# Kernel optimization log

Hardware: AMD Instinct MI355X
Metric: run time of the kernel (lower is better)

The kernel has to match this reference:

```python
import jax, jax.numpy as jnp
import numpy as np

WEIGHT = 0.01

def setup_inputs() -> dict:
    key = jax.random.key(0)
    k1, k2 = jax.random.split(key)
    shape = jax.random.normal(k1, (16, 4096, 3), dtype=jnp.float32)
    template = jax.random.normal(k2, (16, 4096, 3), dtype=jnp.float32)
    return {"shape": shape, "template": template}

def _chamfer(pred, target):
    # Euclidean cdist via the |x|^2 + |y|^2 - 2<x,y> expansion to avoid a (B,M,N,3) tensor.
    p2 = jnp.sum(pred * pred, axis=-1)          # (B, M)
    t2 = jnp.sum(target * target, axis=-1)      # (B, N)
    cross = jnp.einsum('bmd,bnd->bmn', pred, target)  # (B, M, N)
    d2 = p2[:, :, None] + t2[None if p2.ndim == 1 else slice(None), None, :] - 2.0 * cross
    dist = jnp.sqrt(jnp.maximum(d2, 0.0))       # (B, M, N) euclidean, matches torch.cdist
    min_p2t = jnp.min(dist, axis=2)             # (B, M)
    min_t2p = jnp.min(dist, axis=1)             # (B, N)
    chamfer = jnp.sum(min_p2t, axis=1) + jnp.sum(min_t2p, axis=1)  # (B,)
    return jnp.mean(chamfer)                    # reduction='mean'

def reference(shape, template):
    return WEIGHT * _chamfer(shape, template)
```

## Files before the change

kernel.cpp:

```cpp
#include <hip/hip_runtime.h>

#define NPTS 4096
#define NBATCH 16
#define THREADS 256
#define QPB 128
#define TCH 1024
#define NCH (NPTS / TCH)

typedef __attribute__((ext_vector_type(8))) short short8;
typedef __attribute__((ext_vector_type(16))) float float16v;

static __device__ __forceinline__ unsigned short f2bf(float f) {
  unsigned int u = __builtin_bit_cast(unsigned int, f);
  u = (u + 0x7FFFu + ((u >> 16) & 1u)) >> 16;
  return (unsigned short)u;
}
static __device__ __forceinline__ float bf2f(unsigned short h) {
  unsigned int u = ((unsigned int)h) << 16;
  return __builtin_bit_cast(float, u);
}
static __device__ __forceinline__ int toff(int j, int h) {
  return (j * 16 + h * 8) ^ (((j >> 2) & 7) << 3);
}

__global__ __launch_bounds__(THREADS)
__attribute__((amdgpu_waves_per_eu(4, 4)))
void chamfer_mfma(const float* __restrict__ shape,
                  const float* __restrict__ tmpl,
                  float* __restrict__ out) {
  __shared__ unsigned short tgt[TCH * 16];
  __shared__ unsigned short qry[QPB * 16];
  __shared__ float redbuf[4];

  const int qc = blockIdx.x;
  const int b = blockIdx.y;
  const int dir = blockIdx.z;
  const float* Pb = (dir == 0 ? shape : tmpl) + (size_t)b * NPTS * 3;
  const float* Tb = (dir == 0 ? tmpl : shape) + (size_t)b * NPTS * 3;

  const int tid = threadIdx.x;
  const int lane = tid & 63;
  const int wave = tid >> 6;
  const int n = lane & 31;
  const int kg = lane >> 5;

  if (tid < QPB) {
    const int qg = qc * QPB + tid;
    const float px = Pb[3 * qg + 0], py = Pb[3 * qg + 1], pz = Pb[3 * qg + 2];
    const float ux = -2.0f * px, uy = -2.0f * py, uz = -2.0f * pz;
    const float p2 = fmaf(px, px, fmaf(py, py, pz * pz));
    const unsigned short hx = f2bf(ux), hy = f2bf(uy), hz = f2bf(uz);
    const unsigned short lx = f2bf(ux - bf2f(hx)), ly = f2bf(uy - bf2f(hy)),
                         lz = f2bf(uz - bf2f(hz));
    const unsigned short h2 = f2bf(p2), l2 = f2bf(p2 - bf2f(h2));
    const unsigned short ONE = 0x3F80;
    short8 v0, v1;
    v0[0] = hx; v0[1] = hx; v0[2] = lx; v0[3] = hy;
    v0[4] = hy; v0[5] = ly; v0[6] = hz; v0[7] = hz;
    v1[0] = lz; v1[1] = ONE; v1[2] = ONE; v1[3] = h2;
    v1[4] = l2; v1[5] = 0;  v1[6] = 0;  v1[7] = 0;
    *(short8*)&qry[tid * 16] = v0;
    *(short8*)&qry[tid * 16 + 8] = v1;
  }
  __syncthreads();

  const short8 af = *(const short8*)&qry[(wave * 32 + n) * 16 + kg * 8];

  const float INF = 3.402823466e38f;
  float acc[16];
  #pragma unroll
  for (int r = 0; r < 16; ++r) acc[r] = INF;
  const float16v z = {};

  const float4* T4 = (const float4*)Tb;
  for (int ch = 0; ch < NCH; ++ch) {
    __syncthreads();
    {
      const int g = ch * (TCH / 4) + tid;
      const float4 a = T4[g * 3 + 0];
      const float4 c = T4[g * 3 + 1];
      const float4 d = T4[g * 3 + 2];
      const float X[4] = {a.x, a.w, c.z, d.y};
      const float Y[4] = {a.y, c.x, c.w, d.z};
      const float Z[4] = {a.z, c.y, d.x, d.w};
      #pragma unroll
      for (int p = 0; p < 4; ++p) {
        const float x = X[p], y = Y[p], zc = Z[p];
        const float t2 = fmaf(x, x, fmaf(y, y, zc * zc));
        const unsigned short hx = f2bf(x), hy = f2bf(y), hz = f2bf(zc);
        const unsigned short lx = f2bf(x - bf2f(hx)), ly = f2bf(y - bf2f(hy)),
                             lz = f2bf(zc - bf2f(hz));
        const unsigned short h2 = f2bf(t2), l2 = f2bf(t2 - bf2f(h2));
        const unsigned short ONE = 0x3F80;
        short8 v0, v1;
        v0[0] = hx; v0[1] = lx; v0[2] = hx; v0[3] = hy;
        v0[4] = ly; v0[5] = hy; v0[6] = hz; v0[7] = lz;
        v1[0] = hz; v1[1] = h2; v1[2] = l2; v1[3] = ONE;
        v1[4] = ONE; v1[5] = 0; v1[6] = 0; v1[7] = 0;
        const int j = tid * 4 + p;
        *(short8*)&tgt[toff(j, 0)] = v0;
        *(short8*)&tgt[toff(j, 1)] = v1;
      }
    }
    __syncthreads();

    for (int tp = 0; tp < TCH / 64; ++tp) {
      const short8 b0 = *(const short8*)&tgt[toff(tp * 64 + n, kg)];
      const short8 b1 = *(const short8*)&tgt[toff(tp * 64 + 32 + n, kg)];
      float16v d0 = __builtin_amdgcn_mfma_f32_32x32x16_bf16(af, b0, z, 0, 0, 0);
      float16v d1 = __builtin_amdgcn_mfma_f32_32x32x16_bf16(af, b1, z, 0, 0, 0);
      #pragma unroll
      for (int r = 0; r < 16; ++r)
        acc[r] = fminf(fminf(d0[r], d1[r]), acc[r]);
    }
  }

  #pragma unroll
  for (int m = 1; m <= 16; m <<= 1) {
    #pragma unroll
    for (int r = 0; r < 16; ++r)
      acc[r] = fminf(acc[r], __shfl_xor(acc[r], m, 64));
  }

  float s = 0.0f;
  if (n == 0) {
    #pragma unroll
    for (int r = 0; r < 16; ++r)
      s += sqrtf(fmaxf(acc[r], 0.0f));
  }
  s += __shfl_xor(s, 32, 64);
  if (lane == 0) redbuf[wave] = s;
  __syncthreads();
  if (tid == 0) {
    atomicAdd(out, (redbuf[0] + redbuf[1] + redbuf[2] + redbuf[3]) * (0.01f / 16.0f));
  }
}

extern "C" void kernel_launch(void* const* d_in, const int* in_sizes, int n_in,
                              void* d_out, int out_size, void* d_ws, size_t ws_size,
                              hipStream_t stream) {
  const float* shape = (const float*)d_in[0];
  const float* tmpl = (const float*)d_in[1];
  float* out = (float*)d_out;

  hipMemsetAsync(out, 0, sizeof(float) * out_size, stream);

  dim3 grid(NPTS / QPB, NBATCH, 2);
  chamfer_mfma<<<grid, dim3(THREADS), 0, stream>>>(shape, tmpl, out);
}
```

Before: 80.94 us.

## Double queries per wave and split targets across blocks with a finish kernel

Each wave now handles 64 queries with two A fragments, so each B fragment read from LDS feeds four MFMAs instead of two. The target set is split into two halves across grid z, which keeps the block count the same as before. Partial per-query minima are written to workspace and a second kernel combines the halves, takes sqrt and reduces. This trades a second launch, extra global traffic and more accumulator registers for better LDS reuse and less B-conversion work per block.

New measurement: 82.86 us. 2.4% more time.

```diff
diff --git a/kernel.cpp b/kernel.cpp
--- a/kernel.cpp
+++ b/kernel.cpp
@@ -3,9 +3,10 @@
 #define NPTS 4096
 #define NBATCH 16
 #define THREADS 256
-#define QPB 128
+#define QPB 256
+#define TPB 2048
 #define TCH 1024
-#define NCH (NPTS / TCH)
+#define NCH (TPB / TCH)
 
 typedef __attribute__((ext_vector_type(8))) short short8;
 typedef __attribute__((ext_vector_type(16))) float float16v;
@@ -27,14 +28,14 @@
 __attribute__((amdgpu_waves_per_eu(4, 4)))
 void chamfer_mfma(const float* __restrict__ shape,
                   const float* __restrict__ tmpl,
-                  float* __restrict__ out) {
+                  float* __restrict__ ws) {
   __shared__ unsigned short tgt[TCH * 16];
   __shared__ unsigned short qry[QPB * 16];
-  __shared__ float redbuf[4];
 
   const int qc = blockIdx.x;
   const int b = blockIdx.y;
-  const int dir = blockIdx.z;
+  const int dir = blockIdx.z & 1;
+  const int tc = blockIdx.z >> 1;
   const float* Pb = (dir == 0 ? shape : tmpl) + (size_t)b * NPTS * 3;
   const float* Tb = (dir == 0 ? tmpl : shape) + (size_t)b * NPTS * 3;
 
@@ -44,7 +45,7 @@
   const int n = lane & 31;
   const int kg = lane >> 5;
 
-  if (tid < QPB) {
+  {
     const int qg = qc * QPB + tid;
     const float px = Pb[3 * qg + 0], py = Pb[3 * qg + 1], pz = Pb[3 * qg + 2];
     const float ux = -2.0f * px, uy = -2.0f * py, uz = -2.0f * pz;
@@ -64,19 +65,20 @@
   }
   __syncthreads();
 
-  const short8 af = *(const short8*)&qry[(wave * 32 + n) * 16 + kg * 8];
+  const short8 af0 = *(const short8*)&qry[(wave * 64 + n) * 16 + kg * 8];
+  const short8 af1 = *(const short8*)&qry[(wave * 64 + 32 + n) * 16 + kg * 8];
 
   const float INF = 3.402823466e38f;
-  float acc[16];
+  float acc0[16], acc1[16];
   #pragma unroll
-  for (int r = 0; r < 16; ++r) acc[r] = INF;
+  for (int r = 0; r < 16; ++r) { acc0[r] = INF; acc1[r] = INF; }
   const float16v z = {};
 
   const float4* T4 = (const float4*)Tb;
   for (int ch = 0; ch < NCH; ++ch) {
     __syncthreads();
     {
-      const int g = ch * (TCH / 4) + tid;
+      const int g = tc * (TPB / 4) + ch * (TCH / 4) + tid;
       const float4 a = T4[g * 3 + 0];
       const float4 c = T4[g * 3 + 1];
       const float4 d = T4[g * 3 + 2];
@@ -107,33 +109,59 @@
     for (int tp = 0; tp < TCH / 64; ++tp) {
       const short8 b0 = *(const short8*)&tgt[toff(tp * 64 + n, kg)];
       const short8 b1 = *(const short8*)&tgt[toff(tp * 64 + 32 + n, kg)];
-      float16v d0 = __builtin_amdgcn_mfma_f32_32x32x16_bf16(af, b0, z, 0, 0, 0);
-      float16v d1 = __builtin_amdgcn_mfma_f32_32x32x16_bf16(af, b1, z, 0, 0, 0);
+      float16v d0 = __builtin_amdgcn_mfma_f32_32x32x16_bf16(af0, b0, z, 0, 0, 0);
+      float16v d1 = __builtin_amdgcn_mfma_f32_32x32x16_bf16(af0, b1, z, 0, 0, 0);
       #pragma unroll
       for (int r = 0; r < 16; ++r)
-        acc[r] = fminf(fminf(d0[r], d1[r]), acc[r]);
+        acc0[r] = fminf(fminf(d0[r], d1[r]), acc0[r]);
+      float16v d2 = __builtin_amdgcn_mfma_f32_32x32x16_bf16(af1, b0, z, 0, 0, 0);
+      float16v d3 = __builtin_amdgcn_mfma_f32_32x32x16_bf16(af1, b1, z, 0, 0, 0);
+      #pragma unroll
+      for (int r = 0; r < 16; ++r)
+        acc1[r] = fminf(fminf(d2[r], d3[r]), acc1[r]);
     }
   }
 
   #pragma unroll
   for (int m = 1; m <= 16; m <<= 1) {
     #pragma unroll
-    for (int r = 0; r < 16; ++r)
-      acc[r] = fminf(acc[r], __shfl_xor(acc[r], m, 64));
+    for (int r = 0; r < 16; ++r) {
+      acc0[r] = fminf(acc0[r], __shfl_xor(acc0[r], m, 64));
+      acc1[r] = fminf(acc1[r], __shfl_xor(acc1[r], m, 64));
+    }
   }
 
-  float s = 0.0f;
+  float* qmin = (float*)qry;
   if (n == 0) {
     #pragma unroll
-    for (int r = 0; r < 16; ++r)
-      s += sqrtf(fmaxf(acc[r], 0.0f));
+    for (int r = 0; r < 16; ++r) {
+      const int row = (r & 3) + 8 * (r >> 2) + 4 * kg;
+      qmin[wave * 64 + row] = acc0[r];
+      qmin[wave * 64 + 32 + row] = acc1[r];
+    }
   }
-  s += __shfl_xor(s, 32, 64);
-  if (lane == 0) redbuf[wave] = s;
   __syncthreads();
-  if (tid == 0) {
-    atomicAdd(out, (redbuf[0] + redbuf[1] + redbuf[2] + redbuf[3]) * (0.01f / 16.0f));
-  }
+  ws[(size_t)tc * (2 * NBATCH * NPTS) + ((size_t)(dir * NBATCH + b)) * NPTS +
+     qc * QPB + tid] = qmin[tid];
+}
+
+__global__ __launch_bounds__(THREADS)
+void chamfer_finish(const float* __restrict__ ws, float* __restrict__ out) {
+  __shared__ float red[THREADS / 64];
+  const int tid = threadIdx.x;
+  const int i4 = blockIdx.x * THREADS + tid;
+  const float4 a = ((const float4*)ws)[i4];
+  const float4 c = ((const float4*)ws)[(2 * NBATCH * NPTS / 4) + i4];
+  float s = sqrtf(fmaxf(fminf(a.x, c.x), 0.0f)) +
+            sqrtf(fmaxf(fminf(a.y, c.y), 0.0f)) +
+            sqrtf(fmaxf(fminf(a.z, c.z), 0.0f)) +
+            sqrtf(fmaxf(fminf(a.w, c.w), 0.0f));
+  #pragma unroll
+  for (int m = 1; m <= 32; m <<= 1) s += __shfl_xor(s, m, 64);
+  if ((tid & 63) == 0) red[tid >> 6] = s;
+  __syncthreads();
+  if (tid == 0)
+    atomicAdd(out, (red[0] + red[1] + red[2] + red[3]) * (0.01f / 16.0f));
 }
 
 extern "C" void kernel_launch(void* const* d_in, const int* in_sizes, int n_in,
@@ -142,9 +170,11 @@
   const float* shape = (const float*)d_in[0];
   const float* tmpl = (const float*)d_in[1];
   float* out = (float*)d_out;
+  float* ws = (float*)d_ws;
 
   hipMemsetAsync(out, 0, sizeof(float) * out_size, stream);
 
-  dim3 grid(NPTS / QPB, NBATCH, 2);
-  chamfer_mfma<<<grid, dim3(THREADS), 0, stream>>>(shape, tmpl, out);
+  dim3 grid(NPTS / QPB, NBATCH, 4);
+  chamfer_mfma<<<grid, dim3(THREADS), 0, stream>>>(shape, tmpl, ws);
+  chamfer_finish<<<dim3(2 * NBATCH * NPTS / 4 / THREADS), dim3(THREADS), 0, stream>>>(ws, out);
 }
```
